# Optimization experiments

Measured on AMD Instinct MI355X. Metric: run time of the kernel, lower is better.

Reference implementation:

```python
import jax, jax.numpy as jnp
import numpy as np

N = 100_000        # total nodes (BN)
E = 1_600_000      # directed edges before bidirectionalization
B = 8              # graphs in batch
CFG = 1000         # configs per graph -> BC = 8000
N_OPS = 120
OP_EMB = 8
F_NODE = 140
H = 64
IN_DIMS = [F_NODE + OP_EMB, H, H]  # [148, 64, 64]


def setup_inputs() -> dict:
    key = jax.random.key(0)
    ks = iter(jax.random.split(key, 40))
    d = {}
    d["node_feat"] = jax.random.normal(next(ks), (N, F_NODE), dtype=jnp.float32)
    d["node_opcode"] = jax.random.randint(next(ks), (N,), 0, N_OPS)
    d["edge_index"] = jax.random.randint(next(ks), (E, 2), 0, N)
    d["config_feat"] = jax.random.normal(next(ks), (B * CFG, 24), dtype=jnp.float32)
    d["n_configs"] = jnp.full((B,), CFG, dtype=jnp.int32)
    d["batch"] = jnp.repeat(jnp.arange(B, dtype=jnp.int32), N // B)
    d["op_emb"] = jax.random.normal(next(ks), (N_OPS, OP_EMB), dtype=jnp.float32) * 0.1
    s = 0.05
    for l, din in enumerate(IN_DIMS):
        d[f"sage_wl{l}"] = jax.random.normal(next(ks), (din, din), dtype=jnp.float32) * s
        d[f"sage_bl{l}"] = jnp.zeros((din,), dtype=jnp.float32)
        d[f"sage_wr{l}"] = jax.random.normal(next(ks), (din, din), dtype=jnp.float32) * s
        d[f"lin_w{l}"] = jax.random.normal(next(ks), (2 * din, H), dtype=jnp.float32) * s
        d[f"lin_b{l}"] = jnp.zeros((H,), dtype=jnp.float32)
    d["post_w1"] = jax.random.normal(next(ks), (H + 24, H), dtype=jnp.float32) * s
    d["post_b1"] = jnp.zeros((H,), dtype=jnp.float32)
    d["post_w2"] = jax.random.normal(next(ks), (H, 1), dtype=jnp.float32) * s
    d["post_b2"] = jnp.zeros((1,), dtype=jnp.float32)
    return d


def _forward(node_feat, config_feat, op_emb, layer_params, post_w1, post_b1,
             post_w2, post_b2, node_opcode, edge_index, n_configs, batch):
    # Bidirectional edges: original + transposed (matches edge_index[..., [1,0]] cat)
    src = jnp.concatenate([edge_index[:, 0], edge_index[:, 1]])
    dst = jnp.concatenate([edge_index[:, 1], edge_index[:, 0]])
    deg = jax.ops.segment_sum(jnp.ones_like(dst, dtype=node_feat.dtype), dst,
                              num_segments=N)
    inv_deg = (1.0 / jnp.maximum(deg, 1.0))[:, None]  # zero-in-degree -> mean 0

    x = jnp.concatenate([node_feat, op_emb[node_opcode]], axis=-1)  # (N, 148)
    for (wl, bl, wr, lw, lb) in layer_params:
        # SAGEConv: mean-aggregate neighbor messages, + root transform
        agg = jax.ops.segment_sum(x[src], dst, num_segments=N) * inv_deg
        h = agg @ wl + bl + x @ wr
        # normalize=True -> L2 normalize (F.normalize, eps=1e-12)
        nrm = jnp.linalg.norm(h, axis=-1, keepdims=True)
        h = h / jnp.maximum(nrm, 1e-12)
        z = jnp.concatenate([h, x], axis=-1) @ lw + lb
        x = jax.nn.leaky_relu(z)  # negative_slope=0.01 as in torch default

    g = jax.ops.segment_sum(x, batch, num_segments=B)  # global_add_pool (B, 64)
    g = jnp.repeat(g, n_configs, axis=0, total_repeat_length=B * CFG)
    z = jnp.concatenate([g, config_feat], axis=-1)     # (BC, 88)
    z = jax.nn.leaky_relu(z @ post_w1 + post_b1)
    out = (z @ post_w2 + post_b2).squeeze(-1)          # (BC,)
    return out


def reference(node_feat, node_opcode, edge_index, config_feat, n_configs, batch,
              op_emb,
              sage_wl0, sage_bl0, sage_wr0, lin_w0, lin_b0,
              sage_wl1, sage_bl1, sage_wr1, lin_w1, lin_b1,
              sage_wl2, sage_bl2, sage_wr2, lin_w2, lin_b2,
              post_w1, post_b1, post_w2, post_b2):
    layer_params = [
        (sage_wl0, sage_bl0, sage_wr0, lin_w0, lin_b0),
        (sage_wl1, sage_bl1, sage_wr1, lin_w1, lin_b1),
        (sage_wl2, sage_bl2, sage_wr2, lin_w2, lin_b2),
    ]
    return _forward(node_feat, config_feat, op_emb, layer_params,
                    post_w1, post_b1, post_w2, post_b2,
                    node_opcode, edge_index, n_configs, batch)
```

## Files before the change

kernel.cpp:

```cpp
#include <hip/hip_runtime.h>
#include <cstdint>
#include <cstddef>


#define LRELU(v) ((v) > 0.f ? (v) : 0.01f * (v))

typedef __attribute__((ext_vector_type(8))) short bf16x8;
typedef __attribute__((ext_vector_type(4))) float f32x4;
typedef float floatx2 __attribute__((ext_vector_type(2)));

union U4B8 {
    uint4 u;
    bf16x8 b;
};

__device__ inline unsigned bf16_rn(float x) {
    unsigned u = __float_as_uint(x);
    return (u + 0x7fffu + ((u >> 16) & 1u)) >> 16;
}
__device__ inline unsigned pack2(float lo, float hi) {
    return bf16_rn(lo) | (bf16_rn(hi) << 16);
}
__device__ inline float2 up2(unsigned v) {
    return make_float2(__uint_as_float(v << 16), __uint_as_float(v & 0xffff0000u));
}

__device__ inline float e4m3_to_f32(unsigned b) {
    float v = __uint_as_float((b & 0x7fu) << 20) * 0x1p120f;
    return __uint_as_float(__float_as_uint(v) | ((b & 0x80u) << 24));
}

template <bool HI>
__device__ inline floatx2 fp8x2_dec(unsigned v) {
#if __has_builtin(__builtin_amdgcn_cvt_pk_f32_fp8)
    return __builtin_amdgcn_cvt_pk_f32_fp8((int)v, HI);
#else
    unsigned w = HI ? (v >> 16) : v;
    floatx2 r;
    r.x = e4m3_to_f32(w & 0xffu);
    r.y = e4m3_to_f32((w >> 8) & 0xffu);
    return r;
#endif
}

__device__ inline unsigned char f32_to_e4m3_sw(float f) {
    unsigned u = __float_as_uint(f);
    unsigned s = (u >> 24) & 0x80u;
    float a = fabsf(f);
    if (a > 448.f) a = 448.f;
    unsigned b = __float_as_uint(a);
    int exp = (int)(b >> 23) - 127;
    unsigned r;
    if (exp < -9) {
        r = 0;
    } else if (exp >= -6) {
        unsigned m = b & 0x7fffffu;
        unsigned keep = m >> 20;
        unsigned rb = (m >> 19) & 1u;
        unsigned sticky = (m & 0x7ffffu) ? 1u : 0u;
        unsigned inc = rb & (sticky | (keep & 1u));
        unsigned em = (((unsigned)(exp + 7)) << 3) | keep;
        em += inc;
        if (em > 0x7eu) em = 0x7eu;
        r = em;
    } else {
        float t = a * 512.f;
        int q = (int)(t + 0.5f);
        r = (q > 7) ? 0x08u : (unsigned)q;
    }
    return (unsigned char)(r | s);
}

__device__ inline unsigned fp8x4_enc(float f0, float f1, float f2, float f3) {
#if __has_builtin(__builtin_amdgcn_cvt_pk_fp8_f32)
    int pk = __builtin_amdgcn_cvt_pk_fp8_f32(f0, f1, 0, false);
    pk = __builtin_amdgcn_cvt_pk_fp8_f32(f2, f3, pk, true);
    return (unsigned)pk;
#else
    return (unsigned)f32_to_e4m3_sw(f0) | ((unsigned)f32_to_e4m3_sw(f1) << 8) |
           ((unsigned)f32_to_e4m3_sw(f2) << 16) | ((unsigned)f32_to_e4m3_sw(f3) << 24);
#endif
}

__global__ void k_concat(const float* __restrict__ nf, const int* __restrict__ opc,
                         const float* __restrict__ emb, unsigned* __restrict__ x0,
                         unsigned* __restrict__ x8, int n) {
    int idx = blockIdx.x * 256 + threadIdx.x;
    if (idx >= n * 40) return;
    int node = idx / 40;
    int u = idx - node * 40;
    float f[4];
#pragma unroll
    for (int j = 0; j < 4; j++) {
        int ft = 4 * u + j;
        float v = 0.f;
        if (ft < 140) v = nf[(size_t)node * 140 + ft];
        else if (ft < 148) v = emb[opc[node] * 8 + (ft - 140)];
        f[j] = v;
    }
    ((uint2*)x0)[idx] = make_uint2(pack2(f[0], f[1]), pack2(f[2], f[3]));
    x8[idx] = fp8x4_enc(f[0], f[1], f[2], f[3]);
}

__global__ void k_cvt8(const unsigned* __restrict__ xb, unsigned* __restrict__ x8,
                       int n) {
    int idx = blockIdx.x * 256 + threadIdx.x;
    if (idx >= n * 16) return;
    uint2 v = ((const uint2*)xb)[idx];
    float2 ab = up2(v.x);
    float2 cd = up2(v.y);
    x8[idx] = fp8x4_enc(ab.x, ab.y, cd.x, cd.y);
}

__global__ __launch_bounds__(256) void k_bh(const int* __restrict__ ei, int E,
                                            int NBUCK, int* __restrict__ bcnt) {
    __shared__ int h[1024];
    int t = threadIdx.x;
    for (int i = t; i < 1024; i += 256) h[i] = 0;
    __syncthreads();
    int e0 = blockIdx.x * 4096, e1 = min(E, e0 + 4096);
    for (int e = e0 + t; e < e1; e += 256) {
        int a = ei[2 * e], b = ei[2 * e + 1];
        atomicAdd(&h[b >> 7], 1);
        atomicAdd(&h[a >> 7], 1);
    }
    __syncthreads();
    for (int i = t; i < NBUCK; i += 256)
        if (h[i]) atomicAdd(&bcnt[i], h[i]);
}

__global__ void k_bscan(const int* __restrict__ bcnt, int NBUCK,
                        int* __restrict__ bo, int* __restrict__ bfill) {
    __shared__ int sm[1024];
    int t = threadIdx.x;
    int v = (t < NBUCK) ? bcnt[t] : 0;
    sm[t] = v;
    __syncthreads();
    for (int off = 1; off < 1024; off <<= 1) {
        int u = 0;
        if (t >= off) u = sm[t - off];
        __syncthreads();
        sm[t] += u;
        __syncthreads();
    }
    if (t < NBUCK) {
        int ex = sm[t] - v;
        bo[t] = ex;
        bfill[t] = ex;
    }
    if (t == NBUCK - 1) bo[NBUCK] = sm[t];
}

__global__ __launch_bounds__(256) void k_bscatter(const int* __restrict__ ei, int E,
                                                  int* __restrict__ bfill,
                                                  uint2* __restrict__ pairs) {
    __shared__ int hist[1024], lbo[1024], gb[1024], cur[1024];
    __shared__ int wsum[4];
    __shared__ int stageD[8192];
    __shared__ int stageS[8192];
    int t = threadIdx.x;
    for (int i = t; i < 1024; i += 256) hist[i] = 0;
    __syncthreads();
    int e0 = blockIdx.x * 4096, e1 = min(E, e0 + 4096);
    for (int e = e0 + t; e < e1; e += 256) {
        int a = ei[2 * e], b = ei[2 * e + 1];
        atomicAdd(&hist[b >> 7], 1);
        atomicAdd(&hist[a >> 7], 1);
    }
    __syncthreads();
    int b4 = t * 4;
    int c0 = hist[b4], c1 = hist[b4 + 1], c2 = hist[b4 + 2], c3 = hist[b4 + 3];
    int ms = c0 + c1 + c2 + c3;
    int lane = t & 63, wv = t >> 6;
    int v = ms;
#pragma unroll
    for (int off = 1; off < 64; off <<= 1) {
        int u = __shfl_up(v, off, 64);
        if (lane >= off) v += u;
    }
    if (lane == 63) wsum[wv] = v;
    __syncthreads();
    int wb = 0;
    for (int i = 0; i < wv; i++) wb += wsum[i];
    int ex = wb + v - ms;
    lbo[b4] = ex;
    lbo[b4 + 1] = ex + c0;
    lbo[b4 + 2] = ex + c0 + c1;
    lbo[b4 + 3] = ex + c0 + c1 + c2;
    if (c0) gb[b4 + 0] = atomicAdd(&bfill[b4 + 0], c0);
    if (c1) gb[b4 + 1] = atomicAdd(&bfill[b4 + 1], c1);
    if (c2) gb[b4 + 2] = atomicAdd(&bfill[b4 + 2], c2);
    if (c3) gb[b4 + 3] = atomicAdd(&bfill[b4 + 3], c3);
    cur[b4] = 0;
    cur[b4 + 1] = 0;
    cur[b4 + 2] = 0;
    cur[b4 + 3] = 0;
    __syncthreads();
    for (int e = e0 + t; e < e1; e += 256) {
        int a = ei[2 * e], b = ei[2 * e + 1];
        int bk = b >> 7;
        int r = atomicAdd(&cur[bk], 1);
        int p = lbo[bk] + r;
        stageD[p] = b;
        stageS[p] = a;
        bk = a >> 7;
        r = atomicAdd(&cur[bk], 1);
        p = lbo[bk] + r;
        stageD[p] = a;
        stageS[p] = b;
    }
    __syncthreads();
    int tot = 2 * (e1 - e0);
    for (int i = t; i < tot; i += 256) {
        int d = stageD[i];
        int bk = d >> 7;
        pairs[gb[bk] + (i - lbo[bk])] = make_uint2((unsigned)d, (unsigned)stageS[i]);
    }
}

__global__ __launch_bounds__(256) void k_bfinal(const uint2* __restrict__ pairs,
                                                const int* __restrict__ bo,
                                                int* __restrict__ rp,
                                                int* __restrict__ csr,
                                                float* __restrict__ invd,
                                                int N, int NBUCK) {
    __shared__ int hist[128], ls[128], cur[128];
    __shared__ unsigned outS[6144];
    int t = threadIdx.x;
    int bk = blockIdx.x;
    int n0 = bk << 7;
    int nn = min(128, N - n0);
    int base = bo[bk], cnt = bo[bk + 1] - base;
    if (t < 128) {
        hist[t] = 0;
        cur[t] = 0;
    }
    __syncthreads();
    for (int i = t; i < cnt; i += 256) atomicAdd(&hist[(int)pairs[base + i].x - n0], 1);
    __syncthreads();
    if (t == 0) {
        int run = 0;
        for (int i = 0; i < 128; i++) {
            ls[i] = run;
            run += hist[i];
        }
    }
    __syncthreads();
    if (t < nn) {
        int node = n0 + t;
        rp[node] = base + ls[t];
        invd[node] = 1.0f / fmaxf((float)hist[t], 1.0f);
    }
    if (bk == NBUCK - 1 && t == 0) rp[N] = base + cnt;
    bool inl = (cnt <= 6144);
    for (int i = t; i < cnt; i += 256) {
        uint2 pr = pairs[base + i];
        int loc = (int)pr.x - n0;
        int r = atomicAdd(&cur[loc], 1);
        int pos = ls[loc] + r;
        if (inl) outS[pos] = pr.y;
        else csr[base + pos] = (int)pr.y;
    }
    __syncthreads();
    if (inl)
        for (int i = t; i < cnt; i += 256) csr[base + i] = (int)outS[i];
}

__global__ __launch_bounds__(256) void k_agg160(
    const unsigned* __restrict__ x8, const int* __restrict__ rp,
    const int* __restrict__ csr, const float* __restrict__ invd,
    unsigned* __restrict__ agg, int n) {
    int wave = threadIdx.x >> 6;
    int l = threadIdx.x & 63;
    int node = blockIdx.x * 4 + wave;
    if (node >= n) return;
    int p = l & 31;
    int h = l >> 5;
    int eg = l >> 3;
    int eq = l & 7;
    float am[4] = {0.f, 0.f, 0.f, 0.f};
    float ae[4] = {0.f, 0.f, 0.f, 0.f};
    int s = rp[node], e2 = rp[node + 1];
    int j = s;
    for (; j + 8 <= e2; j += 8) {
#pragma unroll
        for (int i = 0; i < 4; i++) {
            int u = csr[j + 2 * i + h];
            unsigned v = x8[(size_t)u * 40 + p];
            floatx2 lo = fp8x2_dec<false>(v);
            floatx2 hi = fp8x2_dec<true>(v);
            am[0] += lo.x;
            am[1] += lo.y;
            am[2] += hi.x;
            am[3] += hi.y;
        }
        int ue = csr[j + eg];
        unsigned v = x8[(size_t)ue * 40 + 32 + eq];
        floatx2 lo = fp8x2_dec<false>(v);
        floatx2 hi = fp8x2_dec<true>(v);
        ae[0] += lo.x;
        ae[1] += lo.y;
        ae[2] += hi.x;
        ae[3] += hi.y;
    }
    for (; j < e2; j++) {
        int u = csr[j];
        if (l < 32) {
            unsigned v = x8[(size_t)u * 40 + p];
            floatx2 lo = fp8x2_dec<false>(v);
            floatx2 hi = fp8x2_dec<true>(v);
            am[0] += lo.x;
            am[1] += lo.y;
            am[2] += hi.x;
            am[3] += hi.y;
        } else if (l < 40) {
            unsigned v = x8[(size_t)u * 40 + 32 + eq];
            floatx2 lo = fp8x2_dec<false>(v);
            floatx2 hi = fp8x2_dec<true>(v);
            ae[0] += lo.x;
            ae[1] += lo.y;
            ae[2] += hi.x;
            ae[3] += hi.y;
        }
    }
#pragma unroll
    for (int r = 0; r < 4; r++) am[r] += __shfl_xor(am[r], 32, 64);
#pragma unroll
    for (int r = 0; r < 4; r++) {
        ae[r] += __shfl_xor(ae[r], 8, 64);
        ae[r] += __shfl_xor(ae[r], 16, 64);
        ae[r] += __shfl_xor(ae[r], 32, 64);
    }
    float iv = invd[node];
    unsigned* row = agg + (size_t)node * 80;
    if (l < 32)
        ((uint2*)row)[p] = make_uint2(pack2(am[0] * iv, am[1] * iv),
                                      pack2(am[2] * iv, am[3] * iv));
    if (l < 8)
        ((uint2*)(row + 64))[eq] = make_uint2(pack2(ae[0] * iv, ae[1] * iv),
                                              pack2(ae[2] * iv, ae[3] * iv));
}

__global__ __launch_bounds__(256) void k_agg64_8(
    const unsigned* __restrict__ x8, const int* __restrict__ rp,
    const int* __restrict__ csr, const float* __restrict__ invd,
    unsigned* __restrict__ agg, int n) {
    int wave = threadIdx.x >> 6;
    int l = threadIdx.x & 63;
    int node = blockIdx.x * 4 + wave;
    if (node >= n) return;
    int p = l & 15;
    int g = l >> 4;
    float a[4] = {0.f, 0.f, 0.f, 0.f};
    int s = rp[node], e2 = rp[node + 1];
    int j = s;
    for (; j + 8 <= e2; j += 8) {
        int u0 = csr[j + g];
        int u1 = csr[j + 4 + g];
        unsigned v0 = x8[(size_t)u0 * 16 + p];
        unsigned v1 = x8[(size_t)u1 * 16 + p];
        floatx2 lo0 = fp8x2_dec<false>(v0);
        floatx2 hi0 = fp8x2_dec<true>(v0);
        floatx2 lo1 = fp8x2_dec<false>(v1);
        floatx2 hi1 = fp8x2_dec<true>(v1);
        a[0] += lo0.x + lo1.x;
        a[1] += lo0.y + lo1.y;
        a[2] += hi0.x + hi1.x;
        a[3] += hi0.y + hi1.y;
    }
    for (; j < e2; j += 4) {
        if (j + g < e2) {
            int u = csr[j + g];
            unsigned v = x8[(size_t)u * 16 + p];
            floatx2 lo = fp8x2_dec<false>(v);
            floatx2 hi = fp8x2_dec<true>(v);
            a[0] += lo.x;
            a[1] += lo.y;
            a[2] += hi.x;
            a[3] += hi.y;
        }
    }
#pragma unroll
    for (int r = 0; r < 4; r++) {
        a[r] += __shfl_xor(a[r], 16, 64);
        a[r] += __shfl_xor(a[r], 32, 64);
    }
    if (l < 16) {
        float iv = invd[node];
        ((uint2*)(agg + (size_t)node * 32))[p] =
            make_uint2(pack2(a[0] * iv, a[1] * iv), pack2(a[2] * iv, a[3] * iv));
    }
}

template <int KS, int KSH, int CT, int C>
__global__ void k_prep(const float* __restrict__ W1, const float* __restrict__ W2,
                       int K1, int K2, uint4* __restrict__ Wp) {
    int idx = blockIdx.x * 256 + threadIdx.x;
    if (idx >= CT * KS * 64) return;
    int l = idx & 63;
    int ks = (idx >> 6) % KS;
    int ct = idx / (KS * 64);
    int col = ct * 16 + (l & 15);
    int kbase = ks * 32 + (l >> 4) * 8;
    unsigned short v[8];
#pragma unroll
    for (int j = 0; j < 8; j++) {
        int k = kbase + j;
        float f = 0.f;
        if (col < C) {
            if (k < KSH * 32) {
                if (k < K1) f = W1[(size_t)k * C + col];
            } else {
                int k2 = k - KSH * 32;
                if (k2 < K2) f = W2[(size_t)k2 * C + col];
            }
        }
        v[j] = (unsigned short)bf16_rn(f);
    }
    uint4 o;
    o.x = v[0] | ((unsigned)v[1] << 16);
    o.y = v[2] | ((unsigned)v[3] << 16);
    o.z = v[4] | ((unsigned)v[5] << 16);
    o.w = v[6] | ((unsigned)v[7] << 16);
    Wp[idx] = o;
}

template <int KS, int KSH, int CT, int C, int OST, int NORM, int ACT, int OUTF>
__global__ __launch_bounds__(256) void k_gemm(
    const uint4* __restrict__ A, const uint4* __restrict__ Bb,
    const uint4* __restrict__ Wp, const float* __restrict__ bias,
    void* __restrict__ outv, int n) {
    int l = threadIdx.x & 63;
    int wv = threadIdx.x >> 6;
    int rb = blockIdx.x * 64 + wv * 16;
    int rowA = rb + (l & 15);
    if (rowA >= n) rowA = n - 1;
    int koct = l >> 4;
    const int strideU = KSH * 4;
    size_t baseA = (size_t)rowA * strideU + koct;

    f32x4 acc[CT];
#pragma unroll
    for (int ct = 0; ct < CT; ct++) acc[ct] = (f32x4){0.f, 0.f, 0.f, 0.f};

#pragma unroll
    for (int ks = 0; ks < KS; ks++) {
        U4B8 a;
        a.u = (ks < KSH) ? A[baseA + ks * 4] : Bb[baseA + (ks - KSH) * 4];
#pragma unroll
        for (int ct = 0; ct < CT; ct++) {
            U4B8 b;
            b.u = Wp[(ct * KS + ks) * 64 + l];
            acc[ct] = __builtin_amdgcn_mfma_f32_16x16x32_bf16(a.b, b.b, acc[ct], 0, 0, 0);
        }
    }

    int cid = l & 15;
    int grp = l >> 4;
#pragma unroll
    for (int ct = 0; ct < CT; ct++) {
        int col = ct * 16 + cid;
        float bv = (col < C) ? bias[col] : 0.f;
#pragma unroll
        for (int r = 0; r < 4; r++) acc[ct][r] += bv;
    }

    if (NORM) {
        float ss[4];
#pragma unroll
        for (int r = 0; r < 4; r++) {
            ss[r] = 0.f;
#pragma unroll
            for (int ct = 0; ct < CT; ct++) ss[r] += acc[ct][r] * acc[ct][r];
        }
#pragma unroll
        for (int off = 1; off < 16; off <<= 1) {
#pragma unroll
            for (int r = 0; r < 4; r++) ss[r] += __shfl_xor(ss[r], off, 64);
        }
#pragma unroll
        for (int r = 0; r < 4; r++) {
            float sc = 1.0f / fmaxf(sqrtf(ss[r]), 1e-12f);
#pragma unroll
            for (int ct = 0; ct < CT; ct++) acc[ct][r] *= sc;
        }
    }

    if (ACT) {
#pragma unroll
        for (int ct = 0; ct < CT; ct++)
#pragma unroll
            for (int r = 0; r < 4; r++) acc[ct][r] = LRELU(acc[ct][r]);
    }

#pragma unroll
    for (int r = 0; r < 4; r++) {
        int row = rb + grp * 4 + r;
        if (row >= n) continue;
        if (OUTF) {
            float* o = (float*)outv;
#pragma unroll
            for (int ct = 0; ct < CT; ct++) {
                int col = ct * 16 + cid;
                if (col < OST) o[(size_t)row * OST + col] = acc[ct][r];
            }
        } else {
            unsigned short* o = (unsigned short*)outv;
#pragma unroll
            for (int ct = 0; ct < CT; ct++) {
                int col = ct * 16 + cid;
                if (col < OST) o[(size_t)row * OST + col] = (unsigned short)bf16_rn(acc[ct][r]);
            }
        }
    }
}

__global__ __launch_bounds__(256) void k_pool(const float* __restrict__ x,
                                              const int* __restrict__ batch,
                                              float* __restrict__ g, int n) {
    __shared__ float sm[8][64];
    __shared__ int sb[8];
    int lane = threadIdx.x & 63;
    int wv = threadIdx.x >> 6;
    int base = blockIdx.x * 256 + wv * 64;
    float a0 = 0.f, a1 = 0.f;
    int b0 = -1, b1 = -1;
    int end = (base + 64 < n) ? base + 64 : n;
    for (int row = base; row < end; row++) {
        int bg = batch[row];
        float v = x[(size_t)row * 64 + lane];
        if (b0 < 0) b0 = bg;
        if (bg == b0) a0 += v;
        else { if (b1 < 0) b1 = bg; a1 += v; }
    }
    sm[wv * 2 + 0][lane] = a0;
    sm[wv * 2 + 1][lane] = a1;
    if (lane == 0) {
        sb[wv * 2 + 0] = b0;
        sb[wv * 2 + 1] = b1;
    }
    __syncthreads();
    if (wv == 0) {
        float c0 = 0.f, c1 = 0.f;
        int d0 = -1, d1 = -1;
#pragma unroll
        for (int s = 0; s < 8; s++) {
            int bg = sb[s];
            if (bg < 0) continue;
            float v = sm[s][lane];
            if (d0 < 0) d0 = bg;
            if (bg == d0) c0 += v;
            else { if (d1 < 0) d1 = bg; c1 += v; }
        }
        if (d0 >= 0) atomicAdd(&g[d0 * 64 + lane], c0);
        if (d1 >= 0) atomicAdd(&g[d1 * 64 + lane], c1);
    }
}

__global__ void k_post1(const float* __restrict__ g, const float* __restrict__ cf,
                        const int* __restrict__ ncfg, const float* __restrict__ w1,
                        const float* __restrict__ b1, float* __restrict__ z,
                        int BC, int B) {
    int idx = blockIdx.x * 256 + threadIdx.x;
    if (idx >= BC * 64) return;
    int row = idx >> 6, c = idx & 63;
    int gsum = 0, gid = B - 1;
    for (int b2 = 0; b2 < B; b2++) {
        int ns = ncfg[b2];
        if (row < gsum + ns) { gid = b2; break; }
        gsum += ns;
    }
    float acc = b1[c];
#pragma unroll 4
    for (int k = 0; k < 64; k++) acc += g[gid * 64 + k] * w1[k * 64 + c];
#pragma unroll 4
    for (int k = 0; k < 24; k++) acc += cf[(size_t)row * 24 + k] * w1[(64 + k) * 64 + c];
    z[idx] = LRELU(acc);
}

__global__ void k_post2(const float* __restrict__ z, const float* __restrict__ w2,
                        const float* __restrict__ b2, float* __restrict__ out, int BC) {
    int row = blockIdx.x * 4 + (threadIdx.x >> 6);
    if (row >= BC) return;
    int c = threadIdx.x & 63;
    float v = z[(size_t)row * 64 + c] * w2[c];
#pragma unroll
    for (int off = 32; off > 0; off >>= 1) v += __shfl_xor(v, off, 64);
    if (c == 0) out[row] = v + b2[0];
}

extern "C" void kernel_launch(void* const* d_in, const int* in_sizes, int n_in,
                              void* d_out, int out_size, void* d_ws, size_t ws_size,
                              hipStream_t stream) {
    const float* node_feat = (const float*)d_in[0];
    const int*   opcode    = (const int*)d_in[1];
    const int*   ei        = (const int*)d_in[2];
    const float* cf        = (const float*)d_in[3];
    const int*   ncfg      = (const int*)d_in[4];
    const int*   batch     = (const int*)d_in[5];
    const float* emb       = (const float*)d_in[6];
    const float* wl0 = (const float*)d_in[7];
    const float* bl0 = (const float*)d_in[8];
    const float* wr0 = (const float*)d_in[9];
    const float* lw0 = (const float*)d_in[10];
    const float* lb0 = (const float*)d_in[11];
    const float* wl1 = (const float*)d_in[12];
    const float* bl1 = (const float*)d_in[13];
    const float* wr1 = (const float*)d_in[14];
    const float* lw1 = (const float*)d_in[15];
    const float* lb1 = (const float*)d_in[16];
    const float* wl2 = (const float*)d_in[17];
    const float* bl2 = (const float*)d_in[18];
    const float* wr2 = (const float*)d_in[19];
    const float* lw2 = (const float*)d_in[20];
    const float* lb2 = (const float*)d_in[21];
    const float* pw1 = (const float*)d_in[22];
    const float* pb1 = (const float*)d_in[23];
    const float* pw2 = (const float*)d_in[24];
    const float* pb2 = (const float*)d_in[25];

    const int N  = in_sizes[0] / 140;
    const int E  = in_sizes[2] / 2;
    const int B  = in_sizes[4];
    const int BC = in_sizes[3] / 24;
    const int NBUCK = (N + 127) >> 7;

    char* w = (char*)d_ws;
    auto alloc = [&](size_t bytes) {
        void* p = (void*)w;
        w += (bytes + 255) & ~(size_t)255;
        return p;
    };
    int*      bcnt     = (int*)alloc(1024 * 4);
    int*      bo       = (int*)alloc(1025 * 4);
    int*      bfill    = (int*)alloc(1024 * 4);
    uint2*    pairs    = (uint2*)alloc((size_t)2 * E * 8);
    int*      rp       = (int*)alloc((size_t)(N + 1) * 4);
    float*    invd     = (float*)alloc((size_t)N * 4);
    int*      csr      = (int*)alloc((size_t)2 * E * 4);
    unsigned* X0       = (unsigned*)alloc((size_t)N * 80 * 4);
    unsigned* AG0      = (unsigned*)alloc((size_t)N * 80 * 4);
    unsigned* H0       = (unsigned*)alloc((size_t)N * 80 * 4);
    unsigned* T0       = (unsigned*)alloc((size_t)N * 32 * 4);
    unsigned* T1       = (unsigned*)alloc((size_t)N * 32 * 4);
    unsigned* T2       = (unsigned*)alloc((size_t)N * 32 * 4);
    unsigned* G8       = (unsigned*)alloc((size_t)N * 16 * 4);
    float*    X3F      = (float*)alloc((size_t)N * 64 * 4);
    float*    gbuf     = (float*)alloc((size_t)B * 64 * 4);
    float*    zp       = (float*)alloc((size_t)BC * 64 * 4);
    uint4*    Wp0h     = (uint4*)alloc((size_t)10 * 10 * 64 * 16);
    uint4*    Wp0l     = (uint4*)alloc((size_t)4 * 10 * 64 * 16);
    uint4*    Wp1h     = (uint4*)alloc((size_t)4 * 4 * 64 * 16);
    uint4*    Wp1l     = (uint4*)alloc((size_t)4 * 4 * 64 * 16);
    uint4*    Wp2h     = (uint4*)alloc((size_t)4 * 4 * 64 * 16);
    uint4*    Wp2l     = (uint4*)alloc((size_t)4 * 4 * 64 * 16);
    unsigned* X08      = (unsigned*)pairs;
    (void)ws_size; (void)n_in; (void)out_size;

    (void)hipMemsetAsync(bcnt, 0, 1024 * 4, stream);
    (void)hipMemsetAsync(gbuf, 0, (size_t)B * 64 * 4, stream);

    k_prep<10, 5, 10, 148><<<(6400 + 255) / 256, 256, 0, stream>>>(wl0, wr0, 148, 148, Wp0h);
    k_prep<10, 5, 4, 64><<<(2560 + 255) / 256, 256, 0, stream>>>(lw0, lw0 + 148 * 64, 148, 148, Wp0l);
    k_prep<4, 2, 4, 64><<<4, 256, 0, stream>>>(wl1, wr1, 64, 64, Wp1h);
    k_prep<4, 2, 4, 64><<<4, 256, 0, stream>>>(lw1, lw1 + 64 * 64, 64, 64, Wp1l);
    k_prep<4, 2, 4, 64><<<4, 256, 0, stream>>>(wl2, wr2, 64, 64, Wp2h);
    k_prep<4, 2, 4, 64><<<4, 256, 0, stream>>>(lw2, lw2 + 64 * 64, 64, 64, Wp2l);

    const int EB = (E + 4095) / 4096;
    k_bh<<<EB, 256, 0, stream>>>(ei, E, NBUCK, bcnt);
    k_bscan<<<1, 1024, 0, stream>>>(bcnt, NBUCK, bo, bfill);
    k_bscatter<<<EB, 256, 0, stream>>>(ei, E, bfill, pairs);
    k_bfinal<<<NBUCK, 256, 0, stream>>>(pairs, bo, rp, csr, invd, N, NBUCK);

    k_concat<<<(N * 40 + 255) / 256, 256, 0, stream>>>(node_feat, opcode, emb, X0, X08, N);

    const int AGG_GRID  = (N + 3) / 4;
    const int GEMM_GRID = (N + 63) / 64;
    const int CVT_GRID  = (N * 16 + 255) / 256;

    k_agg160<<<AGG_GRID, 256, 0, stream>>>(X08, rp, csr, invd, AG0, N);
    k_gemm<10, 5, 10, 148, 160, 1, 0, 0><<<GEMM_GRID, 256, 0, stream>>>(
        (const uint4*)AG0, (const uint4*)X0, Wp0h, bl0, H0, N);
    k_gemm<10, 5, 4, 64, 64, 0, 1, 0><<<GEMM_GRID, 256, 0, stream>>>(
        (const uint4*)H0, (const uint4*)X0, Wp0l, lb0, T0, N);

    k_cvt8<<<CVT_GRID, 256, 0, stream>>>(T0, G8, N);
    k_agg64_8<<<AGG_GRID, 256, 0, stream>>>(G8, rp, csr, invd, T1, N);
    k_gemm<4, 2, 4, 64, 64, 1, 0, 0><<<GEMM_GRID, 256, 0, stream>>>(
        (const uint4*)T1, (const uint4*)T0, Wp1h, bl1, T2, N);
    k_gemm<4, 2, 4, 64, 64, 0, 1, 0><<<GEMM_GRID, 256, 0, stream>>>(
        (const uint4*)T2, (const uint4*)T0, Wp1l, lb1, T1, N);

    k_cvt8<<<CVT_GRID, 256, 0, stream>>>(T1, G8, N);
    k_agg64_8<<<AGG_GRID, 256, 0, stream>>>(G8, rp, csr, invd, T0, N);
    k_gemm<4, 2, 4, 64, 64, 1, 0, 0><<<GEMM_GRID, 256, 0, stream>>>(
        (const uint4*)T0, (const uint4*)T1, Wp2h, bl2, T2, N);
    k_gemm<4, 2, 4, 64, 64, 0, 1, 1><<<GEMM_GRID, 256, 0, stream>>>(
        (const uint4*)T2, (const uint4*)T1, Wp2l, lb2, X3F, N);

    k_pool<<<(N + 255) / 256, 256, 0, stream>>>(X3F, batch, gbuf, N);
    k_post1<<<(BC * 64 + 255) / 256, 256, 0, stream>>>(gbuf, cf, ncfg, pw1, pb1, zp, BC, B);
    k_post2<<<(BC + 3) / 4, 256, 0, stream>>>(zp, pw2, pb2, (float*)d_out, BC);
}
```

Before: 531.3 us.

## Split neighbor aggregation into column-chunk passes to shrink gather footprint

```diff
diff --git a/kernel.cpp b/kernel.cpp
--- a/kernel.cpp
+++ b/kernel.cpp
@@ -266,99 +266,25 @@
         for (int i = t; i < cnt; i += 256) csr[base + i] = (int)outS[i];
 }
 
-__global__ __launch_bounds__(256) void k_agg160(
+template <int XSTR, int OSTR>
+__global__ __launch_bounds__(256) void k_aggc(
     const unsigned* __restrict__ x8, const int* __restrict__ rp,
     const int* __restrict__ csr, const float* __restrict__ invd,
-    unsigned* __restrict__ agg, int n) {
+    uint2* __restrict__ agg, int n, int off) {
     int wave = threadIdx.x >> 6;
     int l = threadIdx.x & 63;
     int node = blockIdx.x * 4 + wave;
     if (node >= n) return;
-    int p = l & 31;
-    int h = l >> 5;
-    int eg = l >> 3;
-    int eq = l & 7;
-    float am[4] = {0.f, 0.f, 0.f, 0.f};
-    float ae[4] = {0.f, 0.f, 0.f, 0.f};
-    int s = rp[node], e2 = rp[node + 1];
-    int j = s;
-    for (; j + 8 <= e2; j += 8) {
-#pragma unroll
-        for (int i = 0; i < 4; i++) {
-            int u = csr[j + 2 * i + h];
-            unsigned v = x8[(size_t)u * 40 + p];
-            floatx2 lo = fp8x2_dec<false>(v);
-            floatx2 hi = fp8x2_dec<true>(v);
-            am[0] += lo.x;
-            am[1] += lo.y;
-            am[2] += hi.x;
-            am[3] += hi.y;
-        }
-        int ue = csr[j + eg];
-        unsigned v = x8[(size_t)ue * 40 + 32 + eq];
-        floatx2 lo = fp8x2_dec<false>(v);
-        floatx2 hi = fp8x2_dec<true>(v);
-        ae[0] += lo.x;
-        ae[1] += lo.y;
-        ae[2] += hi.x;
-        ae[3] += hi.y;
-    }
-    for (; j < e2; j++) {
-        int u = csr[j];
-        if (l < 32) {
-            unsigned v = x8[(size_t)u * 40 + p];
-            floatx2 lo = fp8x2_dec<false>(v);
-            floatx2 hi = fp8x2_dec<true>(v);
-            am[0] += lo.x;
-            am[1] += lo.y;
-            am[2] += hi.x;
-            am[3] += hi.y;
-        } else if (l < 40) {
-            unsigned v = x8[(size_t)u * 40 + 32 + eq];
-            floatx2 lo = fp8x2_dec<false>(v);
-            floatx2 hi = fp8x2_dec<true>(v);
-            ae[0] += lo.x;
-            ae[1] += lo.y;
-            ae[2] += hi.x;
-            ae[3] += hi.y;
-        }
-    }
-#pragma unroll
-    for (int r = 0; r < 4; r++) am[r] += __shfl_xor(am[r], 32, 64);
-#pragma unroll
-    for (int r = 0; r < 4; r++) {
-        ae[r] += __shfl_xor(ae[r], 8, 64);
-        ae[r] += __shfl_xor(ae[r], 16, 64);
-        ae[r] += __shfl_xor(ae[r], 32, 64);
-    }
-    float iv = invd[node];
-    unsigned* row = agg + (size_t)node * 80;
-    if (l < 32)
-        ((uint2*)row)[p] = make_uint2(pack2(am[0] * iv, am[1] * iv),
-                                      pack2(am[2] * iv, am[3] * iv));
-    if (l < 8)
-        ((uint2*)(row + 64))[eq] = make_uint2(pack2(ae[0] * iv, ae[1] * iv),
-                                              pack2(ae[2] * iv, ae[3] * iv));
-}
-
-__global__ __launch_bounds__(256) void k_agg64_8(
-    const unsigned* __restrict__ x8, const int* __restrict__ rp,
-    const int* __restrict__ csr, const float* __restrict__ invd,
-    unsigned* __restrict__ agg, int n) {
-    int wave = threadIdx.x >> 6;
-    int l = threadIdx.x & 63;
-    int node = blockIdx.x * 4 + wave;
-    if (node >= n) return;
-    int p = l & 15;
-    int g = l >> 4;
+    int c = l & 7;
+    int q = l >> 3;
     float a[4] = {0.f, 0.f, 0.f, 0.f};
     int s = rp[node], e2 = rp[node + 1];
     int j = s;
-    for (; j + 8 <= e2; j += 8) {
-        int u0 = csr[j + g];
-        int u1 = csr[j + 4 + g];
-        unsigned v0 = x8[(size_t)u0 * 16 + p];
-        unsigned v1 = x8[(size_t)u1 * 16 + p];
+    for (; j + 16 <= e2; j += 16) {
+        int u0 = csr[j + q];
+        int u1 = csr[j + 8 + q];
+        unsigned v0 = x8[(size_t)u0 * XSTR + off + c];
+        unsigned v1 = x8[(size_t)u1 * XSTR + off + c];
         floatx2 lo0 = fp8x2_dec<false>(v0);
         floatx2 hi0 = fp8x2_dec<true>(v0);
         floatx2 lo1 = fp8x2_dec<false>(v1);
@@ -368,10 +294,10 @@
         a[2] += hi0.x + hi1.x;
         a[3] += hi0.y + hi1.y;
     }
-    for (; j < e2; j += 4) {
-        if (j + g < e2) {
-            int u = csr[j + g];
-            unsigned v = x8[(size_t)u * 16 + p];
+    for (; j < e2; j += 8) {
+        if (j + q < e2) {
+            int u = csr[j + q];
+            unsigned v = x8[(size_t)u * XSTR + off + c];
             floatx2 lo = fp8x2_dec<false>(v);
             floatx2 hi = fp8x2_dec<true>(v);
             a[0] += lo.x;
@@ -382,12 +308,13 @@
     }
 #pragma unroll
     for (int r = 0; r < 4; r++) {
+        a[r] += __shfl_xor(a[r], 8, 64);
         a[r] += __shfl_xor(a[r], 16, 64);
         a[r] += __shfl_xor(a[r], 32, 64);
     }
-    if (l < 16) {
+    if (l < 8) {
         float iv = invd[node];
-        ((uint2*)(agg + (size_t)node * 32))[p] =
+        agg[(size_t)node * OSTR + off + c] =
             make_uint2(pack2(a[0] * iv, a[1] * iv), pack2(a[2] * iv, a[3] * iv));
     }
 }
@@ -679,21 +606,27 @@
     const int GEMM_GRID = (N + 63) / 64;
     const int CVT_GRID  = (N * 16 + 255) / 256;
 
-    k_agg160<<<AGG_GRID, 256, 0, stream>>>(X08, rp, csr, invd, AG0, N);
+    for (int off = 0; off < 40; off += 8)
+        k_aggc<40, 40><<<AGG_GRID, 256, 0, stream>>>(X08, rp, csr, invd,
+                                                     (uint2*)AG0, N, off);
     k_gemm<10, 5, 10, 148, 160, 1, 0, 0><<<GEMM_GRID, 256, 0, stream>>>(
         (const uint4*)AG0, (const uint4*)X0, Wp0h, bl0, H0, N);
     k_gemm<10, 5, 4, 64, 64, 0, 1, 0><<<GEMM_GRID, 256, 0, stream>>>(
         (const uint4*)H0, (const uint4*)X0, Wp0l, lb0, T0, N);
 
     k_cvt8<<<CVT_GRID, 256, 0, stream>>>(T0, G8, N);
-    k_agg64_8<<<AGG_GRID, 256, 0, stream>>>(G8, rp, csr, invd, T1, N);
+    for (int off = 0; off < 16; off += 8)
+        k_aggc<16, 16><<<AGG_GRID, 256, 0, stream>>>(G8, rp, csr, invd,
+                                                     (uint2*)T1, N, off);
     k_gemm<4, 2, 4, 64, 64, 1, 0, 0><<<GEMM_GRID, 256, 0, stream>>>(
         (const uint4*)T1, (const uint4*)T0, Wp1h, bl1, T2, N);
     k_gemm<4, 2, 4, 64, 64, 0, 1, 0><<<GEMM_GRID, 256, 0, stream>>>(
         (const uint4*)T2, (const uint4*)T0, Wp1l, lb1, T1, N);
 
     k_cvt8<<<CVT_GRID, 256, 0, stream>>>(T1, G8, N);
-    k_agg64_8<<<AGG_GRID, 256, 0, stream>>>(G8, rp, csr, invd, T0, N);
+    for (int off = 0; off < 16; off += 8)
+        k_aggc<16, 16><<<AGG_GRID, 256, 0, stream>>>(G8, rp, csr, invd,
+                                                     (uint2*)T0, N, off);
     k_gemm<4, 2, 4, 64, 64, 1, 0, 0><<<GEMM_GRID, 256, 0, stream>>>(
         (const uint4*)T0, (const uint4*)T1, Wp2h, bl2, T2, N);
     k_gemm<4, 2, 4, 64, 64, 0, 1, 1><<<GEMM_GRID, 256, 0, stream>>>(
```

After: 739.3 us. +39.2%, slower.
